# Performance work log

Hardware: AMD Instinct MI355X
Metric: run time of the kernel (lower is better)

## Reference

```python
import jax, jax.numpy as jnp
import numpy as np

D_MODEL = 256
NHEAD = 4
HEAD_DIM = D_MODEL // NHEAD
TEMP = float(np.sqrt(D_MODEL / NHEAD))
EPS = 1e-5


def layernorm(x, g, b):
    mu = jnp.mean(x, axis=-1, keepdims=True)
    var = jnp.mean(jnp.square(x - mu), axis=-1, keepdims=True)
    return (x - mu) * jax.lax.rsqrt(var + EPS) * g + b


def setup_inputs() -> dict:
    key = jax.random.key(0)
    ks = jax.random.split(key, 8)
    B, S, D = 4, 4096, D_MODEL
    s = 1.0 / np.sqrt(D)
    return {
        "x": jax.random.normal(ks[0], (B, S, D), dtype=jnp.float32),
        "Wq": jax.random.normal(ks[1], (D, D), dtype=jnp.float32) * s,
        "Wk": jax.random.normal(ks[2], (D, D), dtype=jnp.float32) * s,
        "Wv": jax.random.normal(ks[3], (D, D), dtype=jnp.float32) * s,
        "g1": jnp.ones((D,), jnp.float32),
        "b1": jnp.zeros((D,), jnp.float32),
        "g2": jnp.ones((D,), jnp.float32),
        "b2": jnp.zeros((D,), jnp.float32),
        "W1": jax.random.normal(ks[4], (D, D), dtype=jnp.float32) * s,
        "bf1": jnp.zeros((D,), jnp.float32),
        "W2": jax.random.normal(ks[5], (D, D), dtype=jnp.float32) * s,
        "bf2": jnp.zeros((D,), jnp.float32),
    }


def reference(x, Wq, Wk, Wv, g1, b1, g2, b2, W1, bf1, W2, bf2):
    B, S, D = x.shape
    xn = layernorm(x, g1, b1)
    # torch Linear (no bias): y = x @ W.T
    q = (xn @ Wq.T).reshape(B, S, NHEAD, HEAD_DIM)
    k = (xn @ Wk.T).reshape(B, S, NHEAD, HEAD_DIM)
    v = (xn @ Wv.T).reshape(B, S, NHEAD, HEAD_DIM)
    scores = jnp.einsum("bqhd,bkhd->bhqk", q, k) / TEMP
    causal = jnp.tril(jnp.ones((S, S), dtype=bool))  # True = keep
    scores = jnp.where(causal, scores, -jnp.inf)
    attn = jax.nn.softmax(scores, axis=-1)
    att = jnp.einsum("bhqk,bkhd->bqhd", attn, v).reshape(B, S, D)
    xt = x + att
    h = layernorm(xt, g2, b2)
    ffn = jax.nn.relu(h @ W1.T + bf1) @ W2.T + bf2
    return xt + ffn
```

## Files before the change

kernel.cpp:

```cpp
#include <hip/hip_runtime.h>
#include <math.h>

#define D_MODEL 256
#define NHEAD 4
#define HEAD_DIM 64
#define SEQ 4096
#define BATCH 4
#define MROWS (BATCH * SEQ)

typedef __attribute__((ext_vector_type(8))) short short8;
typedef __attribute__((ext_vector_type(4))) short short4v;
typedef __attribute__((ext_vector_type(8))) __bf16 bf16x8;
typedef __attribute__((ext_vector_type(4))) float f32x4;

__device__ inline short f2bf(float f) {
  unsigned u = __float_as_uint(f);
  u += 0x7fffu + ((u >> 16) & 1u);
  return (short)(u >> 16);
}
__device__ inline bf16x8 as_bf8(short8 s) {
  union { short8 s; bf16x8 b; } u;
  u.s = s;
  return u.b;
}
__device__ __forceinline__ void g2lds16(const void* g, void* l) {
  __builtin_amdgcn_global_load_lds(
      (const __attribute__((address_space(1))) unsigned int*)g,
      (__attribute__((address_space(3))) unsigned int*)l, 16, 0, 0);
}

__device__ __forceinline__ f32x4 mfma16bf(short4v a, short4v b, f32x4 c) {
#if __has_builtin(__builtin_amdgcn_mfma_f32_16x16x16bf16_1k)
  return __builtin_amdgcn_mfma_f32_16x16x16bf16_1k(a, b, c, 0, 0, 0);
#else
  asm("v_mfma_f32_16x16x16_bf16 %0, %1, %2, %0" : "+v"(c) : "v"(a), "v"(b));
  return c;
#endif
}

#define QSCALE 0.1803368801111204f

__global__ __launch_bounds__(256) void wcvt(const float* __restrict__ s0, const float* __restrict__ s1,
                                            const float* __restrict__ s2, const float* __restrict__ s3,
                                            const float* __restrict__ s4, short* __restrict__ d0,
                                            short* __restrict__ d1, short* __restrict__ d2,
                                            short* __restrict__ d3, short* __restrict__ d4) {
  int mat = blockIdx.x >> 5;
  int e = ((blockIdx.x & 31) * 256 + threadIdx.x) * 8;
  const float* s = mat == 0 ? s0 : mat == 1 ? s1 : mat == 2 ? s2 : mat == 3 ? s3 : s4;
  short* d = mat == 0 ? d0 : mat == 1 ? d1 : mat == 2 ? d2 : mat == 3 ? d3 : d4;
  int n = e >> 8, k0 = e & 255;
  float4 f0 = *(const float4*)(s + n * 256 + k0);
  float4 f1 = *(const float4*)(s + n * 256 + k0 + 4);
  short8 o = {f2bf(f0.x), f2bf(f0.y), f2bf(f0.z), f2bf(f0.w),
              f2bf(f1.x), f2bf(f1.y), f2bf(f1.z), f2bf(f1.w)};
  int chunk = k0 >> 5, g = (k0 >> 3) & 3;
  *(short8*)(d + n * 256 + chunk * 32 + ((g ^ (n & 3)) * 8)) = o;
}

__global__ __launch_bounds__(256) void ln_sw(const float* __restrict__ x,
                                             const float* __restrict__ g,
                                             const float* __restrict__ b,
                                             short* __restrict__ o) {
  int r = threadIdx.x >> 5, c8 = threadIdx.x & 31;
  int row = blockIdx.x * 8 + r;
  const float* xr = x + (size_t)row * D_MODEL + c8 * 8;
  float4 a = *(const float4*)xr;
  float4 c = *(const float4*)(xr + 4);
  float s = a.x + a.y + a.z + a.w + c.x + c.y + c.z + c.w;
#pragma unroll
  for (int off = 16; off > 0; off >>= 1) s += __shfl_xor(s, off);
  float mu = s * (1.0f / D_MODEL);
  float d0 = a.x - mu, d1 = a.y - mu, d2 = a.z - mu, d3 = a.w - mu;
  float d4 = c.x - mu, d5 = c.y - mu, d6 = c.z - mu, d7 = c.w - mu;
  float ss = d0 * d0 + d1 * d1 + d2 * d2 + d3 * d3 + d4 * d4 + d5 * d5 + d6 * d6 + d7 * d7;
#pragma unroll
  for (int off = 16; off > 0; off >>= 1) ss += __shfl_xor(ss, off);
  float rstd = rsqrtf(ss * (1.0f / D_MODEL) + 1e-5f);
  float4 ga = *(const float4*)(g + c8 * 8);
  float4 gc = *(const float4*)(g + c8 * 8 + 4);
  float4 ba = *(const float4*)(b + c8 * 8);
  float4 bc = *(const float4*)(b + c8 * 8 + 4);
  short8 ov = {f2bf(d0 * rstd * ga.x + ba.x), f2bf(d1 * rstd * ga.y + ba.y),
               f2bf(d2 * rstd * ga.z + ba.z), f2bf(d3 * rstd * ga.w + ba.w),
               f2bf(d4 * rstd * gc.x + bc.x), f2bf(d5 * rstd * gc.y + bc.y),
               f2bf(d6 * rstd * gc.z + bc.z), f2bf(d7 * rstd * gc.w + bc.w)};
  int chunk = c8 >> 2, gr = c8 & 3;
  *(short8*)(o + (size_t)row * D_MODEL + chunk * 32 + ((gr ^ (row & 3)) * 8)) = ov;
}

__global__ __launch_bounds__(256) void qkv_direct(
    const short* __restrict__ Wqi, const short* __restrict__ Wki,
    const short* __restrict__ Wvi, const short* __restrict__ Xn,
    short* __restrict__ qo, short* __restrict__ kimg, short* __restrict__ vimg) {
  __shared__ __align__(16) short Xs[64 * 256];
  const int t = threadIdx.x, lane = t & 63, w = t >> 6;
  const int l15 = lane & 15, quad = lane >> 4;
  const int m0 = blockIdx.x * 64;
  const int which = blockIdx.y;
  const short* Wb = which == 0 ? Wqi : which == 1 ? Wki : Wvi;

#pragma unroll
  for (int j = 0; j < 8; j++) {
    int so = __builtin_amdgcn_readfirstlane((w * 8 + j) * 512);
    g2lds16(Xn + (size_t)m0 * D_MODEL + so + lane * 8, &Xs[so]);
  }
  __syncthreads();

  const short* xb = &Xs[l15 * 256 + ((quad ^ (l15 & 3)) * 8)];
  const short* wb = Wb + (size_t)(w * 64 + l15) * 256 + ((quad ^ (l15 & 3)) * 8);

  f32x4 acc[4][4];
#pragma unroll
  for (int i = 0; i < 4; i++)
#pragma unroll
    for (int j = 0; j < 4; j++) acc[i][j] = (f32x4){0.f, 0.f, 0.f, 0.f};

#pragma unroll
  for (int kf = 0; kf < 8; kf++) {
    bf16x8 fx[4], fw[4];
#pragma unroll
    for (int i = 0; i < 4; i++) {
      fx[i] = as_bf8(*(const short8*)(xb + i * 4096 + kf * 32));
      fw[i] = as_bf8(*(const short8*)(wb + i * 4096 + kf * 32));
    }
    if (which == 2) {
#pragma unroll
      for (int mt = 0; mt < 4; mt++)
#pragma unroll
        for (int nt = 0; nt < 4; nt++)
          acc[mt][nt] = __builtin_amdgcn_mfma_f32_16x16x32_bf16(fx[mt], fw[nt], acc[mt][nt], 0, 0, 0);
    } else {
#pragma unroll
      for (int mt = 0; mt < 4; mt++)
#pragma unroll
        for (int nt = 0; nt < 4; nt++)
          acc[mt][nt] = __builtin_amdgcn_mfma_f32_16x16x32_bf16(fw[nt], fx[mt], acc[mt][nt], 0, 0, 0);
    }
  }

#pragma unroll
  for (int mt = 0; mt < 4; mt++)
#pragma unroll
    for (int nt = 0; nt < 4; nt++) {
      f32x4 v = acc[mt][nt];
      if (which == 2) {
        int n = w * 64 + nt * 16 + l15;
        int mr = m0 + mt * 16 + quad * 4;
        int b = mr >> 12, s = mr & 4095, h = n >> 6, d = n & 63;
        size_t off = ((size_t)(b * NHEAD + h) * 64 + (s >> 6)) * 4096 +
                     (size_t)d * 64 + ((((s & 63) >> 3) ^ (d & 7)) * 8) + (s & 7);
        short4v o = {f2bf(v[0]), f2bf(v[1]), f2bf(v[2]), f2bf(v[3])};
        *(short4v*)(vimg + off) = o;
      } else {
        int m = m0 + mt * 16 + l15;
        int nb = w * 64 + nt * 16 + quad * 4;
        if (which == 0) {
          v *= QSCALE;
          short4v o = {f2bf(v[0]), f2bf(v[1]), f2bf(v[2]), f2bf(v[3])};
          *(short4v*)(qo + (size_t)m * D_MODEL + nb) = o;
        } else {
          int b = m >> 12, s = m & 4095, h = nb >> 6, d = nb & 63;
          size_t off = ((size_t)(b * NHEAD + h) * 64 + (s >> 6)) * 4096 +
                       (size_t)(s & 63) * 64 + (((d >> 3) ^ (s & 7)) * 8) + (d & 7);
          short4v o = {f2bf(v[0]), f2bf(v[1]), f2bf(v[2]), f2bf(v[3])};
          *(short4v*)(kimg + off) = o;
        }
      }
    }
}

__global__ __launch_bounds__(256) void ffn_direct(
    const short* __restrict__ w1i, const short* __restrict__ w2i,
    const short* __restrict__ Hsw, const float* __restrict__ bf1,
    const float* __restrict__ bf2, const float* __restrict__ xt,
    float* __restrict__ out) {
  __shared__ __align__(16) short Hs[32 * 256];
  __shared__ __align__(16) short F1s[32 * 264];
  const int t = threadIdx.x, lane = t & 63, w = t >> 6;
  const int l15 = lane & 15, quad = lane >> 4;
  const int m0 = blockIdx.x * 32;

#pragma unroll
  for (int j = 0; j < 4; j++) {
    int so = __builtin_amdgcn_readfirstlane((w * 4 + j) * 512);
    g2lds16(Hsw + (size_t)m0 * D_MODEL + so + lane * 8, &Hs[so]);
  }
  __syncthreads();

  const short* hb = &Hs[l15 * 256 + ((quad ^ (l15 & 3)) * 8)];
  const short* w1b = w1i + (size_t)(w * 64 + l15) * 256 + ((quad ^ (l15 & 3)) * 8);
  const short* w2b = w2i + (size_t)(w * 64 + l15) * 256 + ((quad ^ (l15 & 3)) * 8);

  f32x4 a1[2][4];
#pragma unroll
  for (int i = 0; i < 2; i++)
#pragma unroll
    for (int j = 0; j < 4; j++) a1[i][j] = (f32x4){0.f, 0.f, 0.f, 0.f};
#pragma unroll
  for (int kf = 0; kf < 8; kf++) {
    bf16x8 fh[2], fw1[4];
#pragma unroll
    for (int i = 0; i < 2; i++) fh[i] = as_bf8(*(const short8*)(hb + i * 4096 + kf * 32));
#pragma unroll
    for (int i = 0; i < 4; i++) fw1[i] = as_bf8(*(const short8*)(w1b + i * 4096 + kf * 32));
#pragma unroll
    for (int mt = 0; mt < 2; mt++)
#pragma unroll
      for (int nt = 0; nt < 4; nt++)
        a1[mt][nt] = __builtin_amdgcn_mfma_f32_16x16x32_bf16(fw1[nt], fh[mt], a1[mt][nt], 0, 0, 0);
  }
#pragma unroll
  for (int mt = 0; mt < 2; mt++)
#pragma unroll
    for (int nt = 0; nt < 4; nt++) {
      int n1 = w * 64 + nt * 16 + quad * 4;
      int ml = mt * 16 + l15;
      float4 bv = *(const float4*)(bf1 + n1);
      f32x4 v = a1[mt][nt];
      short4v o = {f2bf(fmaxf(v[0] + bv.x, 0.f)), f2bf(fmaxf(v[1] + bv.y, 0.f)),
                   f2bf(fmaxf(v[2] + bv.z, 0.f)), f2bf(fmaxf(v[3] + bv.w, 0.f))};
      *(short4v*)&F1s[ml * 264 + n1] = o;
    }
  __syncthreads();

  const short* fb = &F1s[l15 * 264 + quad * 8];
  f32x4 a2[2][4];
#pragma unroll
  for (int i = 0; i < 2; i++)
#pragma unroll
    for (int j = 0; j < 4; j++) a2[i][j] = (f32x4){0.f, 0.f, 0.f, 0.f};
#pragma unroll
  for (int kf = 0; kf < 8; kf++) {
    bf16x8 ff[2], fw2[4];
#pragma unroll
    for (int i = 0; i < 2; i++) ff[i] = as_bf8(*(const short8*)(fb + i * 16 * 264 + kf * 32));
#pragma unroll
    for (int i = 0; i < 4; i++) fw2[i] = as_bf8(*(const short8*)(w2b + i * 4096 + kf * 32));
#pragma unroll
    for (int mt = 0; mt < 2; mt++)
#pragma unroll
      for (int nt = 0; nt < 4; nt++)
        a2[mt][nt] = __builtin_amdgcn_mfma_f32_16x16x32_bf16(ff[mt], fw2[nt], a2[mt][nt], 0, 0, 0);
  }
#pragma unroll
  for (int mt = 0; mt < 2; mt++)
#pragma unroll
    for (int nt = 0; nt < 4; nt++) {
      int n2 = w * 64 + nt * 16 + l15;
      int mg = m0 + mt * 16 + quad * 4;
      float bv = bf2[n2];
      f32x4 v = a2[mt][nt];
#pragma unroll
      for (int r = 0; r < 4; r++) {
        size_t a = (size_t)(mg + r) * D_MODEL + n2;
        out[a] = v[r] + bv + xt[a];
      }
    }
}

__global__ __launch_bounds__(256) void attn_v6(const short* __restrict__ qb,
                                               const short* __restrict__ kimg,
                                               const short* __restrict__ vimg,
                                               const float* __restrict__ x,
                                               float* __restrict__ xt) {
  __shared__ __align__(16) short Ks[2 * 4096];
  __shared__ __align__(16) short Vs[2 * 4096];

  const int t = threadIdx.x, lane = t & 63, w = t >> 6;
  const int quad = lane >> 4, l15 = lane & 15, l7 = lane & 7;
  const int yy = blockIdx.y, gq = yy >> 4, rq = yy & 15;
  const int qt = gq == 0 ? 63 - rq : gq == 1 ? rq : gq == 2 ? 47 - rq : 16 + rq;
  const int bh = blockIdx.x, b = bh >> 2, h = bh & 3;
  const int ldsoff = __builtin_amdgcn_readfirstlane(w * 512);
  const short* kb_bh = kimg + (size_t)bh * 64 * 4096;
  const short* vb_bh = vimg + (size_t)bh * 64 * 4096;

  const short* kb0 = &Ks[l15 * 64 + ((quad ^ l7) * 8)];
  const short* kb1 = &Ks[l15 * 64 + (((4 + quad) ^ l7) * 8)];
  const short* vbase = &Vs[l15 * 64 + ((quad & 1) * 4)];
  const int q1 = quad >> 1;

  const int q0 = qt * 64;
  const int qrow = q0 + w * 16 + l15;
  const int wq_lo = q0 + w * 16, wq_hi = wq_lo + 15;

  bf16x8 qf0, qf1;
  {
    const short* qp = qb + ((size_t)(b * SEQ + qrow)) * D_MODEL + h * HEAD_DIM + quad * 8;
    qf0 = as_bf8(*(const short8*)qp);
    qf1 = as_bf8(*(const short8*)(qp + 32));
  }
  f32x4 oacc[4];
#pragma unroll
  for (int i = 0; i < 4; i++) oacc[i] = (f32x4){0.f, 0.f, 0.f, 0.f};
  float lrun = 0.f;

  const int niter = (qt + 2) >> 1;

#pragma unroll
  for (int i = 0; i < 4; i++) {
    g2lds16(kb_bh + i * 2048 + t * 8, &Ks[i * 2048 + ldsoff]);
    g2lds16(vb_bh + i * 2048 + t * 8, &Vs[i * 2048 + ldsoff]);
  }
  __syncthreads();

  for (int it = 0; it < niter; it++) {
    const int j0 = it * 128;

    const bool half1 = (j0 + 64) <= wq_hi;
    const int kcmax = half1 ? 8 : 4;
    f32x4 st[8];
#pragma unroll
    for (int kc = 0; kc < 8; kc++) {
      if (kc < kcmax) {
        f32x4 z = (f32x4){0.f, 0.f, 0.f, 0.f};
        bf16x8 kf0 = as_bf8(*(const short8*)(kb0 + (kc & 3) * 1024 + (kc >> 2) * 4096));
        bf16x8 kf1 = as_bf8(*(const short8*)(kb1 + (kc & 3) * 1024 + (kc >> 2) * 4096));
        z = __builtin_amdgcn_mfma_f32_16x16x32_bf16(kf0, qf0, z, 0, 0, 0);
        z = __builtin_amdgcn_mfma_f32_16x16x32_bf16(kf1, qf1, z, 0, 0, 0);
        st[kc] = z;
      }
    }
    if (j0 + 127 > wq_lo) {
#pragma unroll
      for (int kc = 0; kc < 8; kc++)
        if (kc < kcmax) {
#pragma unroll
          for (int r = 0; r < 4; r++)
            if (j0 + kc * 16 + quad * 4 + r > qrow) st[kc][r] = -1e30f;
        }
    }
    uint2 pu[8];
#pragma unroll
    for (int kc = 0; kc < 8; kc++) {
      if (kc < kcmax) {
        float p0 = __builtin_amdgcn_exp2f(st[kc][0]);
        float p1 = __builtin_amdgcn_exp2f(st[kc][1]);
        float p2 = __builtin_amdgcn_exp2f(st[kc][2]);
        float p3 = __builtin_amdgcn_exp2f(st[kc][3]);
        lrun += p0 + p1 + p2 + p3;
        pu[kc].x = (__float_as_uint(p0) >> 16) | (__float_as_uint(p1) & 0xffff0000u);
        pu[kc].y = (__float_as_uint(p2) >> 16) | (__float_as_uint(p3) & 0xffff0000u);
      }
    }

    __syncthreads();

    if (it + 1 < niter) {
      const short* kc_base = kb_bh + (size_t)(2 * (it + 1)) * 4096;
#pragma unroll
      for (int i = 0; i < 4; i++)
        g2lds16(kc_base + i * 2048 + t * 8, &Ks[i * 2048 + ldsoff]);
    }

#pragma unroll
    for (int kc = 0; kc < 8; kc++) {
      if (kc < kcmax) {
        union { uint2 u; short4v s; } pb;
        pb.u = pu[kc];
        const short* vk = vbase + (kc >> 2) * 4096 + (((((kc & 3) * 2) | q1) ^ l7) * 8);
#pragma unroll
        for (int dt = 0; dt < 4; dt++) {
          short4v vv = *(const short4v*)(vk + dt * 1024);
          oacc[dt] = mfma16bf(vv, pb.s, oacc[dt]);
        }
      }
    }

    __syncthreads();

    if (it + 1 < niter) {
      const short* vc_base = vb_bh + (size_t)(2 * (it + 1)) * 4096;
#pragma unroll
      for (int i = 0; i < 4; i++)
        g2lds16(vc_base + i * 2048 + t * 8, &Vs[i * 2048 + ldsoff]);
    }
  }

  lrun += __shfl_xor(lrun, 16);
  lrun += __shfl_xor(lrun, 32);
  float inv = 1.0f / lrun;
  size_t rowb = ((size_t)(b * SEQ + qrow)) * D_MODEL + h * HEAD_DIM;
#pragma unroll
  for (int dt = 0; dt < 4; dt++) {
    size_t a = rowb + dt * 16 + quad * 4;
    float4 xv = *(const float4*)(x + a);
    float4 o = make_float4(oacc[dt][0] * inv + xv.x, oacc[dt][1] * inv + xv.y,
                           oacc[dt][2] * inv + xv.z, oacc[dt][3] * inv + xv.w);
    *(float4*)(xt + a) = o;
  }
}

extern "C" void kernel_launch(void* const* d_in, const int* in_sizes, int n_in,
                              void* d_out, int out_size, void* d_ws,
                              size_t ws_size, hipStream_t stream) {
  const float* x = (const float*)d_in[0];
  const float* Wq = (const float*)d_in[1];
  const float* Wk = (const float*)d_in[2];
  const float* Wv = (const float*)d_in[3];
  const float* g1 = (const float*)d_in[4];
  const float* b1 = (const float*)d_in[5];
  const float* g2 = (const float*)d_in[6];
  const float* b2 = (const float*)d_in[7];
  const float* W1 = (const float*)d_in[8];
  const float* bf1 = (const float*)d_in[9];
  const float* W2 = (const float*)d_in[10];
  const float* bf2 = (const float*)d_in[11];
  float* out = (float*)d_out;

  char* ws = (char*)d_ws;
  float* xt = (float*)ws;
  short* q_bf = (short*)(ws + (16u << 20));
  short* kimg = (short*)(ws + (24u << 20));
  short* vimg = (short*)(ws + (32u << 20));
  short* xn_sw = (short*)(ws + (40u << 20));
  short* wq_i = (short*)(ws + (48u << 20));
  short* wk_i = wq_i + 65536;
  short* wv_i = wq_i + 2 * 65536;
  short* w1_i = wq_i + 3 * 65536;
  short* w2_i = wq_i + 4 * 65536;

  dim3 blk(256);
  wcvt<<<160, blk, 0, stream>>>(Wq, Wk, Wv, W1, W2, wq_i, wk_i, wv_i, w1_i, w2_i);
  ln_sw<<<MROWS / 8, blk, 0, stream>>>(x, g1, b1, xn_sw);
  qkv_direct<<<dim3(MROWS / 64, 3), blk, 0, stream>>>(wq_i, wk_i, wv_i, xn_sw,
                                                      q_bf, kimg, vimg);
  attn_v6<<<dim3(16, 64), blk, 0, stream>>>(q_bf, kimg, vimg, x, xt);
  ln_sw<<<MROWS / 8, blk, 0, stream>>>(xt, g2, b2, xn_sw);
  ffn_direct<<<MROWS / 32, blk, 0, stream>>>(w1_i, w2_i, xn_sw, bf1, bf2, xt, out);
}
```

Before: 199.3 us.

## Split attention work across waves by key instead of by query rows

The attention kernel now has each wave handle all 64 query rows of the tile against its own 32-key slice of each 128-key chunk, rather than 16 query rows against every key. Each K/V fragment read from LDS is reused across four query sub-tiles, which cuts LDS traffic per MFMA, and causally masked key slices are skipped per wave. The partial outputs and row sums are then reduced across the four waves through shared memory in a round-robin, adding extra barriers and an LDS reduction phase. Register pressure rises (16 accumulators), and launch bounds request 3 blocks per SIMD.

```diff
diff --git a/kernel.cpp b/kernel.cpp
--- a/kernel.cpp
+++ b/kernel.cpp
@@ -259,16 +259,17 @@
     }
 }
 
-__global__ __launch_bounds__(256) void attn_v6(const short* __restrict__ qb,
-                                               const short* __restrict__ kimg,
-                                               const short* __restrict__ vimg,
-                                               const float* __restrict__ x,
-                                               float* __restrict__ xt) {
+__global__ __launch_bounds__(256, 3) void attn_v7(const short* __restrict__ qb,
+                                                  const short* __restrict__ kimg,
+                                                  const short* __restrict__ vimg,
+                                                  const float* __restrict__ x,
+                                                  float* __restrict__ xt) {
   __shared__ __align__(16) short Ks[2 * 4096];
   __shared__ __align__(16) short Vs[2 * 4096];
 
   const int t = threadIdx.x, lane = t & 63, w = t >> 6;
   const int quad = lane >> 4, l15 = lane & 15, l7 = lane & 7;
+  const int qa = quad & 1, q1 = quad >> 1;
   const int yy = blockIdx.y, gq = yy >> 4, rq = yy & 15;
   const int qt = gq == 0 ? 63 - rq : gq == 1 ? rq : gq == 2 ? 47 - rq : 16 + rq;
   const int bh = blockIdx.x, b = bh >> 2, h = bh & 3;
@@ -276,25 +277,38 @@
   const short* kb_bh = kimg + (size_t)bh * 64 * 4096;
   const short* vb_bh = vimg + (size_t)bh * 64 * 4096;
 
-  const short* kb0 = &Ks[l15 * 64 + ((quad ^ l7) * 8)];
-  const short* kb1 = &Ks[l15 * 64 + (((4 + quad) ^ l7) * 8)];
-  const short* vbase = &Vs[l15 * 64 + ((quad & 1) * 4)];
-  const int q1 = quad >> 1;
-
+  const int sb = w * 32;
   const int q0 = qt * 64;
-  const int qrow = q0 + w * 16 + l15;
-  const int wq_lo = q0 + w * 16, wq_hi = wq_lo + 15;
-
-  bf16x8 qf0, qf1;
+
+  const short* ka[2][2];
+#pragma unroll
+  for (int kk = 0; kk < 2; kk++)
+#pragma unroll
+    for (int dh = 0; dh < 2; dh++)
+      ka[kk][dh] = &Ks[(sb + kk * 16 + l15) * 64 + (((quad + 4 * dh) ^ l7) * 8)];
+  const short* va[2];
+#pragma unroll
+  for (int kk = 0; kk < 2; kk++) {
+    int sk = sb + kk * 16;
+    va[kk] = &Vs[(sk >> 6) * 4096 + l15 * 64 + ((((((sk & 63) >> 3) | q1) ^ l7)) * 8) + qa * 4];
+  }
+
+  bf16x8 qf[4][2];
   {
-    const short* qp = qb + ((size_t)(b * SEQ + qrow)) * D_MODEL + h * HEAD_DIM + quad * 8;
-    qf0 = as_bf8(*(const short8*)qp);
-    qf1 = as_bf8(*(const short8*)(qp + 32));
-  }
-  f32x4 oacc[4];
-#pragma unroll
-  for (int i = 0; i < 4; i++) oacc[i] = (f32x4){0.f, 0.f, 0.f, 0.f};
-  float lrun = 0.f;
+    const short* qpb = qb + ((size_t)(b * SEQ + q0 + l15)) * D_MODEL + h * HEAD_DIM + quad * 8;
+#pragma unroll
+    for (int qq = 0; qq < 4; qq++) {
+      qf[qq][0] = as_bf8(*(const short8*)(qpb + qq * 16 * D_MODEL));
+      qf[qq][1] = as_bf8(*(const short8*)(qpb + qq * 16 * D_MODEL + 32));
+    }
+  }
+
+  f32x4 oacc[4][4];
+#pragma unroll
+  for (int i = 0; i < 4; i++)
+#pragma unroll
+    for (int j = 0; j < 4; j++) oacc[i][j] = (f32x4){0.f, 0.f, 0.f, 0.f};
+  float lrun[4] = {0.f, 0.f, 0.f, 0.f};
 
   const int niter = (qt + 2) >> 1;
 
@@ -307,42 +321,48 @@
 
   for (int it = 0; it < niter; it++) {
     const int j0 = it * 128;
-
-    const bool half1 = (j0 + 64) <= wq_hi;
-    const int kcmax = half1 ? 8 : 4;
-    f32x4 st[8];
-#pragma unroll
-    for (int kc = 0; kc < 8; kc++) {
-      if (kc < kcmax) {
-        f32x4 z = (f32x4){0.f, 0.f, 0.f, 0.f};
-        bf16x8 kf0 = as_bf8(*(const short8*)(kb0 + (kc & 3) * 1024 + (kc >> 2) * 4096));
-        bf16x8 kf1 = as_bf8(*(const short8*)(kb1 + (kc & 3) * 1024 + (kc >> 2) * 4096));
-        z = __builtin_amdgcn_mfma_f32_16x16x32_bf16(kf0, qf0, z, 0, 0, 0);
-        z = __builtin_amdgcn_mfma_f32_16x16x32_bf16(kf1, qf1, z, 0, 0, 0);
-        st[kc] = z;
-      }
-    }
-    if (j0 + 127 > wq_lo) {
-#pragma unroll
-      for (int kc = 0; kc < 8; kc++)
-        if (kc < kcmax) {
-#pragma unroll
-          for (int r = 0; r < 4; r++)
-            if (j0 + kc * 16 + quad * 4 + r > qrow) st[kc][r] = -1e30f;
+    const bool active = (j0 + sb) <= (q0 + 63);
+
+    uint2 pu[2][4];
+    if (active) {
+      f32x4 st[2][4];
+#pragma unroll
+      for (int kk = 0; kk < 2; kk++) {
+        bf16x8 k0 = as_bf8(*(const short8*)(ka[kk][0]));
+        bf16x8 k1 = as_bf8(*(const short8*)(ka[kk][1]));
+#pragma unroll
+        for (int qq = 0; qq < 4; qq++) {
+          f32x4 z = (f32x4){0.f, 0.f, 0.f, 0.f};
+          z = __builtin_amdgcn_mfma_f32_16x16x32_bf16(k0, qf[qq][0], z, 0, 0, 0);
+          z = __builtin_amdgcn_mfma_f32_16x16x32_bf16(k1, qf[qq][1], z, 0, 0, 0);
+          st[kk][qq] = z;
         }
-    }
-    uint2 pu[8];
-#pragma unroll
-    for (int kc = 0; kc < 8; kc++) {
-      if (kc < kcmax) {
-        float p0 = __builtin_amdgcn_exp2f(st[kc][0]);
-        float p1 = __builtin_amdgcn_exp2f(st[kc][1]);
-        float p2 = __builtin_amdgcn_exp2f(st[kc][2]);
-        float p3 = __builtin_amdgcn_exp2f(st[kc][3]);
-        lrun += p0 + p1 + p2 + p3;
-        pu[kc].x = (__float_as_uint(p0) >> 16) | (__float_as_uint(p1) & 0xffff0000u);
-        pu[kc].y = (__float_as_uint(p2) >> 16) | (__float_as_uint(p3) & 0xffff0000u);
-      }
+      }
+      if (j0 + sb + 31 > q0) {
+#pragma unroll
+        for (int kk = 0; kk < 2; kk++) {
+          int kbase = j0 + sb + kk * 16 + quad * 4;
+#pragma unroll
+          for (int qq = 0; qq < 4; qq++) {
+            int qrow = q0 + qq * 16 + l15;
+#pragma unroll
+            for (int r = 0; r < 4; r++)
+              if (kbase + r > qrow) st[kk][qq][r] = -1e30f;
+          }
+        }
+      }
+#pragma unroll
+      for (int kk = 0; kk < 2; kk++)
+#pragma unroll
+        for (int qq = 0; qq < 4; qq++) {
+          float p0 = __builtin_amdgcn_exp2f(st[kk][qq][0]);
+          float p1 = __builtin_amdgcn_exp2f(st[kk][qq][1]);
+          float p2 = __builtin_amdgcn_exp2f(st[kk][qq][2]);
+          float p3 = __builtin_amdgcn_exp2f(st[kk][qq][3]);
+          lrun[qq] += p0 + p1 + p2 + p3;
+          pu[kk][qq].x = (__float_as_uint(p0) >> 16) | (__float_as_uint(p1) & 0xffff0000u);
+          pu[kk][qq].y = (__float_as_uint(p2) >> 16) | (__float_as_uint(p3) & 0xffff0000u);
+        }
     }
 
     __syncthreads();
@@ -354,16 +374,21 @@
         g2lds16(kc_base + i * 2048 + t * 8, &Ks[i * 2048 + ldsoff]);
     }
 
-#pragma unroll
-    for (int kc = 0; kc < 8; kc++) {
-      if (kc < kcmax) {
-        union { uint2 u; short4v s; } pb;
-        pb.u = pu[kc];
-        const short* vk = vbase + (kc >> 2) * 4096 + (((((kc & 3) * 2) | q1) ^ l7) * 8);
+    if (active) {
+#pragma unroll
+      for (int kk = 0; kk < 2; kk++) {
+        union { uint2 u; short4v s; } pb0, pb1, pb2, pb3;
+        pb0.u = pu[kk][0];
+        pb1.u = pu[kk][1];
+        pb2.u = pu[kk][2];
+        pb3.u = pu[kk][3];
 #pragma unroll
         for (int dt = 0; dt < 4; dt++) {
-          short4v vv = *(const short4v*)(vk + dt * 1024);
-          oacc[dt] = mfma16bf(vv, pb.s, oacc[dt]);
+          short4v vv = *(const short4v*)(va[kk] + dt * 1024);
+          oacc[dt][0] = mfma16bf(vv, pb0.s, oacc[dt][0]);
+          oacc[dt][1] = mfma16bf(vv, pb1.s, oacc[dt][1]);
+          oacc[dt][2] = mfma16bf(vv, pb2.s, oacc[dt][2]);
+          oacc[dt][3] = mfma16bf(vv, pb3.s, oacc[dt][3]);
         }
       }
     }
@@ -378,18 +403,63 @@
     }
   }
 
-  lrun += __shfl_xor(lrun, 16);
-  lrun += __shfl_xor(lrun, 32);
-  float inv = 1.0f / lrun;
-  size_t rowb = ((size_t)(b * SEQ + qrow)) * D_MODEL + h * HEAD_DIM;
-#pragma unroll
-  for (int dt = 0; dt < 4; dt++) {
-    size_t a = rowb + dt * 16 + quad * 4;
-    float4 xv = *(const float4*)(x + a);
-    float4 o = make_float4(oacc[dt][0] * inv + xv.x, oacc[dt][1] * inv + xv.y,
-                           oacc[dt][2] * inv + xv.z, oacc[dt][3] * inv + xv.w);
-    *(float4*)(xt + a) = o;
-  }
+#pragma unroll
+  for (int qq = 0; qq < 4; qq++) {
+    lrun[qq] += __shfl_xor(lrun[qq], 16);
+    lrun[qq] += __shfl_xor(lrun[qq], 32);
+  }
+  float* ored = (float*)Ks;
+  float* lred = (float*)Vs;
+  __syncthreads();
+  if (quad == 0) {
+#pragma unroll
+    for (int qq = 0; qq < 4; qq++) lred[(w * 4 + qq) * 16 + l15] = lrun[qq];
+  }
+#pragma unroll
+  for (int rr = 1; rr < 4; rr++) {
+#pragma unroll
+    for (int dt = 0; dt < 4; dt++)
+      if (dt == ((w + rr) & 3)) {
+#pragma unroll
+        for (int qq = 0; qq < 4; qq++)
+#pragma unroll
+          for (int e = 0; e < 4; e++)
+            ored[dt * 1024 + (quad * 4 + e) * 64 + qq * 16 + l15] = oacc[dt][qq][e];
+      }
+    __syncthreads();
+#pragma unroll
+    for (int dt = 0; dt < 4; dt++)
+      if (dt == w) {
+#pragma unroll
+        for (int qq = 0; qq < 4; qq++)
+#pragma unroll
+          for (int e = 0; e < 4; e++)
+            oacc[dt][qq][e] += ored[dt * 1024 + (quad * 4 + e) * 64 + qq * 16 + l15];
+      }
+    if (rr < 3) __syncthreads();
+  }
+  float inv[4];
+#pragma unroll
+  for (int qq = 0; qq < 4; qq++) {
+    float s = lred[qq * 16 + l15] + lred[(4 + qq) * 16 + l15] +
+              lred[(8 + qq) * 16 + l15] + lred[(12 + qq) * 16 + l15];
+    inv[qq] = 1.0f / s;
+  }
+#pragma unroll
+  for (int dt = 0; dt < 4; dt++)
+    if (dt == w) {
+      size_t rowb = ((size_t)(b * SEQ + q0 + l15)) * D_MODEL + h * HEAD_DIM + dt * 16 + quad * 4;
+#pragma unroll
+      for (int qq = 0; qq < 4; qq++) {
+        size_t a = rowb + (size_t)qq * 16 * D_MODEL;
+        float4 xv = *(const float4*)(x + a);
+        float4 o = make_float4(oacc[dt][qq][0] * inv[qq] + xv.x,
+                               oacc[dt][qq][1] * inv[qq] + xv.y,
+                               oacc[dt][qq][2] * inv[qq] + xv.z,
+                               oacc[dt][qq][3] * inv[qq] + xv.w);
+        *(float4*)(xt + a) = o;
+      }
+    }
 }
 
 extern "C" void kernel_launch(void* const* d_in, const int* in_sizes, int n_in,
@@ -426,7 +496,7 @@
   ln_sw<<<MROWS / 8, blk, 0, stream>>>(x, g1, b1, xn_sw);
   qkv_direct<<<dim3(MROWS / 64, 3), blk, 0, stream>>>(wq_i, wk_i, wv_i, xn_sw,
                                                       q_bf, kimg, vimg);
-  attn_v6<<<dim3(16, 64), blk, 0, stream>>>(q_bf, kimg, vimg, x, xt);
+  attn_v7<<<dim3(16, 64), blk, 0, stream>>>(q_bf, kimg, vimg, x, xt);
   ln_sw<<<MROWS / 8, blk, 0, stream>>>(xt, g2, b2, xn_sw);
   ffn_direct<<<MROWS / 32, blk, 0, stream>>>(w1_i, w2_i, xn_sw, bf1, bf2, xt, out);
 }
```

Result: faster. 184.8 us (-7.3%).
